# Kernel tuning notes

Measured on AMD Instinct MI355X. Metric: run time of the kernel, lower is better.

## Reference

```python
import jax, jax.numpy as jnp
import numpy as np

T, S, B, E, H = 1024, 1024, 4, 1024, 16
D = E // H          # head_dim = 64
CO = 10             # co_dim fixed in the module


def _xavier(k, shape):
    fan_out, fan_in = shape[0], shape[-1]
    s = (2.0 / (fan_in + fan_out)) ** 0.5
    return jax.random.normal(k, shape, jnp.float32) * s


def setup_inputs() -> dict:
    rng = jax.random.key(0)
    ks = jax.random.split(rng, 12)
    return {
        "query": jax.random.normal(ks[0], (T, B, E), jnp.float32),
        "key": jax.random.normal(ks[1], (S, B, E), jnp.float32),
        "value": jax.random.normal(ks[2], (S, B, E), jnp.float32),
        "in_proj_weight": _xavier(ks[3], (3 * E, E)),
        "in_proj_bias": jnp.zeros((3 * E,), jnp.float32),
        "out_proj_w": _xavier(ks[4], (E, E)),
        "out_proj_b": jnp.zeros((E,), jnp.float32),
        "co_C_q_w": _xavier(ks[5], (D, D)),
        "co_q_w": _xavier(ks[6], (CO, D)),
        "co_k_w": _xavier(ks[7], (CO, D)),
        "h_q_w": _xavier(ks[8], (1, CO)),
        "h_k_w": _xavier(ks[9], (1, CO)),
    }


def reference(query, key, value, in_proj_weight, in_proj_bias,
              out_proj_w, out_proj_b, co_C_q_w, co_q_w, co_k_w,
              h_q_w, h_k_w):
    tgt_len, bsz, embed_dim = query.shape
    src_len = key.shape[0]
    scaling = D ** (-0.5)

    Wq, Wk, Wv = jnp.split(in_proj_weight, 3, axis=0)
    bq, bk, bv = jnp.split(in_proj_bias, 3, axis=0)

    q = (query @ Wq.T + bq) * scaling                 # [T, B, E]
    k = key @ Wk.T + bk                               # [S, B, E]
    v = value @ Wv.T + bv                             # [S, B, E]

    # [T, B*H, D] -> [B*H, T, D]
    q = jnp.transpose(q.reshape(tgt_len, bsz * H, D), (1, 0, 2))
    k = jnp.transpose(k.reshape(src_len, bsz * H, D), (1, 0, 2))
    v = jnp.transpose(v.reshape(src_len, bsz * H, D), (1, 0, 2))

    # ---- co-attention gating ----
    qW = q @ co_C_q_w.T                               # [BH, T, D]
    C = jnp.tanh(jnp.einsum('btd,bsd->bts', qW, k))   # [BH, T, S]

    q2 = q @ co_q_w.T                                 # [BH, T, CO]
    k2 = k @ co_k_w.T                                 # [BH, S, CO]

    # H_q_in = q2^T + k2^T @ C^T : [BH, CO, T]
    H_q = jnp.tanh(jnp.swapaxes(q2, 1, 2) + jnp.einsum('bsc,bts->bct', k2, C))
    # H_k_in = k2^T + q2^T @ C : [BH, CO, S]
    H_k = jnp.tanh(jnp.swapaxes(k2, 1, 2) + jnp.einsum('btc,bts->bcs', q2, C))

    H_q_W = jnp.swapaxes(H_q, 1, 2) @ h_q_w.T         # [BH, T, 1]
    H_k_W = jnp.swapaxes(H_k, 1, 2) @ h_k_w.T         # [BH, S, 1]

    # NOTE: softmax over the last (size-1) axis, as in the original code;
    # this yields all-ones gates but is reproduced faithfully.
    a_q = jax.nn.softmax(H_q_W, axis=-1)              # [BH, T, 1]
    a_k = jax.nn.softmax(H_k_W, axis=-1)              # [BH, S, 1]

    q = q * a_q                                       # broadcast == repeat to D
    k = k * a_k

    # ---- standard attention ----
    attn_weights = jnp.einsum('btd,bsd->bts', q, k)   # [BH, T, S]
    attn_weights = jax.nn.softmax(attn_weights, axis=-1)
    attn = jnp.einsum('bts,bsd->btd', attn_weights, v)  # [BH, T, D]

    attn = jnp.transpose(attn, (1, 0, 2)).reshape(tgt_len, bsz, embed_dim)
    attn = attn @ out_proj_w.T + out_proj_b           # [T, B, E]

    aw = attn_weights.reshape(bsz, H, tgt_len, src_len).sum(axis=1) / H
    return attn, aw
```

## Files before the change

### kernel.cpp

```cpp
#include <hip/hip_runtime.h>

typedef __attribute__((ext_vector_type(8))) short s8v;
typedef __attribute__((ext_vector_type(4))) float f4v;
typedef unsigned short u16;

#define T_LEN 1024
#define B_SZ 4
#define H_NUM 16
#define D_DIM 64
#define E_DIM 1024

#define MBY ((size_t)1<<20)

#define OFF_X(z)     ((size_t)(z)*16*MBY)
#define OFF_AW(g)    ((size_t)(g)*16*MBY)
#define OFF_VT_HI    (32*MBY)
#define OFF_VT_LO    (40*MBY)
#define OFF_ATTN32   (48*MBY)
#define OFF_IPW_HI   (64*MBY)
#define OFF_IPW_LO   (70*MBY)
#define OFF_OPW_HI   (76*MBY)
#define OFF_OPW_LO   (78*MBY)
#define OFF_QKV(z)   ((80*MBY) + (size_t)(z)*16*MBY)
#define OFF_ATTN_HI  (80*MBY)
#define OFF_ATTN_LO  (88*MBY)

__device__ __forceinline__ u16 f2bf(float x){
    unsigned u = __float_as_uint(x);
    u += 0x7fffu + ((u>>16)&1u);
    return (u16)(u>>16);
}
__device__ __forceinline__ float bf2f(u16 h){
    return __uint_as_float(((unsigned)h)<<16);
}
__device__ __forceinline__ void glds16(const void* g, void* l){
    __builtin_amdgcn_global_load_lds((const __attribute__((address_space(1))) unsigned*)g,
                                     (__attribute__((address_space(3))) unsigned*)l, 16, 0, 0);
}
#define MFMA_BF16(a,b,c) __builtin_amdgcn_mfma_f32_16x16x32_bf16((a),(b),(c),0,0,0)

__global__ __launch_bounds__(256) void split_bf16(const float* __restrict__ src,
        u16* __restrict__ hi, u16* __restrict__ lo)
{
    size_t i = ((size_t)blockIdx.x*256 + threadIdx.x)*8;
    float4 a = *(const float4*)(src + i);
    float4 b = *(const float4*)(src + i + 4);
    float v[8] = {a.x,a.y,a.z,a.w,b.x,b.y,b.z,b.w};
    s8v hv, lv;
    #pragma unroll
    for (int j=0;j<8;++j){
        u16 h = f2bf(v[j]);
        hv[j] = (short)h;
        lv[j] = (short)f2bf(v[j] - bf2f(h));
    }
    *(s8v*)(hi+i) = hv;
    *(s8v*)(lo+i) = lv;
}

template<int MODE>
__global__ __launch_bounds__(256) void gemm_split(char* __restrict__ wsb,
        const float* __restrict__ bias0, float* __restrict__ out32)
{
    __shared__ u16 Ah[4096], Al[4096], Bh[4096], Bl[4096];
    const int tid = threadIdx.x;
    const int wv = tid>>6, l = tid&63;
    const int lr = l&15, lg = l>>4;
    const int z = (MODE==0)? blockIdx.z : 0;

    const u16 *Ahi,*Alo,*Whi,*Wlo;
    const float* bias; float scale;
    u16 *outH = nullptr, *outL = nullptr;
    if (MODE==0){
        Ahi = (const u16*)(wsb + OFF_X(z));
        Alo = Ahi + 4*MBY;
        Whi = (const u16*)(wsb + OFF_IPW_HI) + (size_t)z*E_DIM*E_DIM;
        Wlo = (const u16*)(wsb + OFF_IPW_LO) + (size_t)z*E_DIM*E_DIM;
        bias = bias0 + z*E_DIM;
        scale = (z==0)? 0.125f : 1.0f;
        outH = (u16*)(wsb + OFF_QKV(z));
        outL = outH + 4*MBY;
    } else {
        Ahi = (const u16*)(wsb + OFF_ATTN_HI);
        Alo = (const u16*)(wsb + OFF_ATTN_LO);
        Whi = (const u16*)(wsb + OFF_OPW_HI);
        Wlo = (const u16*)(wsb + OFF_OPW_LO);
        bias = bias0; scale = 1.0f;
    }

    const int m0 = blockIdx.y*128, n0 = blockIdx.x*128;

    f4v acc[4][4];
    #pragma unroll
    for (int i=0;i<4;++i)
        #pragma unroll
        for (int j=0;j<4;++j) acc[i][j] = (f4v){0.f,0.f,0.f,0.f};

    for (int k0=0; k0<E_DIM; k0+=32){
        #pragma unroll
        for (int i=0;i<2;++i){
            int ci  = i*4 + wv;
            int row = ci*16 + (l>>2);
            int u   = (l&3) ^ ((l>>2)&3);
            size_t aoff = (size_t)(m0+row)*E_DIM + k0 + u*8;
            size_t boff = (size_t)(n0+row)*E_DIM + k0 + u*8;
            glds16(Ahi+aoff, &Ah[ci*512]);
            glds16(Alo+aoff, &Al[ci*512]);
            glds16(Whi+boff, &Bh[ci*512]);
            glds16(Wlo+boff, &Bl[ci*512]);
        }
        __syncthreads();
        s8v ah[4],al[4],bh[4],bl[4];
        #pragma unroll
        for (int mi=0;mi<4;++mi){
            int row = (wv>>1)*64 + mi*16 + lr;
            int off = row*32 + ((lg ^ (row&3))<<3);
            ah[mi] = *(const s8v*)&Ah[off];
            al[mi] = *(const s8v*)&Al[off];
        }
        #pragma unroll
        for (int ni=0;ni<4;++ni){
            int row = (wv&1)*64 + ni*16 + lr;
            int off = row*32 + ((lg ^ (row&3))<<3);
            bh[ni] = *(const s8v*)&Bh[off];
            bl[ni] = *(const s8v*)&Bl[off];
        }
        #pragma unroll
        for (int mi=0;mi<4;++mi)
            #pragma unroll
            for (int ni=0;ni<4;++ni){
                acc[mi][ni] = MFMA_BF16(ah[mi], bh[ni], acc[mi][ni]);
                acc[mi][ni] = MFMA_BF16(ah[mi], bl[ni], acc[mi][ni]);
                acc[mi][ni] = MFMA_BF16(al[mi], bh[ni], acc[mi][ni]);
            }
        __syncthreads();
    }

    #pragma unroll
    for (int mi=0;mi<4;++mi){
        #pragma unroll
        for (int ni=0;ni<4;++ni){
            int n = n0 + (wv&1)*64 + ni*16 + lr;
            float bn = bias[n];
            #pragma unroll
            for (int r=0;r<4;++r){
                int m = m0 + (wv>>1)*64 + mi*16 + lg*4 + r;
                float val = (acc[mi][ni][r] + bn)*scale;
                if (MODE==0){
                    int t = m>>2, bb = m&3, hh2 = n>>6, dd = n&63;
                    size_t idx = ((size_t)(bb*H_NUM+hh2)*T_LEN + t)*D_DIM + dd;
                    u16 hb_ = f2bf(val);
                    outH[idx] = hb_;
                    outL[idx] = f2bf(val - bf2f(hb_));
                } else {
                    out32[(size_t)m*E_DIM + n] = val;
                }
            }
        }
    }
}

__global__ __launch_bounds__(256) void transpose_v(char* __restrict__ wsb)
{
    __shared__ u16 Th[64][72], Tl[64][72];
    const int tid = threadIdx.x;
    const int bh  = blockIdx.y;
    const int s0  = blockIdx.x*64;
    const u16* vh = (const u16*)(wsb + OFF_QKV(2));
    const u16* vl = vh + 4*MBY;
    u16* th = (u16*)(wsb + OFF_VT_HI);
    u16* tl = (u16*)(wsb + OFF_VT_LO);

    #pragma unroll
    for (int it=0; it<2; ++it){
        int u = it*256 + tid;
        int s = u>>3, c8 = u&7;
        size_t off = ((size_t)bh*T_LEN + s0+s)*D_DIM + c8*8;
        s8v a  = *(const s8v*)&vh[off];
        s8v b_ = *(const s8v*)&vl[off];
        #pragma unroll
        for (int j=0;j<8;++j){
            Th[c8*8+j][s] = (u16)a[j];
            Tl[c8*8+j][s] = (u16)b_[j];
        }
    }
    __syncthreads();
    #pragma unroll
    for (int it=0; it<2; ++it){
        int u = it*256 + tid;
        int d = u>>3, sc = u&7;
        s8v rh = *(const s8v*)&Th[d][sc*8];
        s8v rl = *(const s8v*)&Tl[d][sc*8];
        size_t off = ((size_t)bh*D_DIM + d)*T_LEN + s0 + sc*8;
        *(s8v*)&th[off] = rh;
        *(s8v*)&tl[off] = rl;
    }
}

__global__ __launch_bounds__(256) void attn_mfma(char* __restrict__ wsb)
{
    __shared__ u16 Ph[2][1024], Pl[2][1024];
    __shared__ float redM[16][4], redS[16][4];

    const int tid = threadIdx.x;
    const int wv = tid>>6, l = tid&63, lr = l&15, lg = l>>4;
    const int t0 = blockIdx.x*16;
    const int hg = blockIdx.y;
    const int b  = blockIdx.z;

    const u16* qhi = (const u16*)(wsb + OFF_QKV(0));
    const u16* qlo = qhi + 4*MBY;
    const u16* khi = (const u16*)(wsb + OFF_QKV(1));
    const u16* klo = khi + 4*MBY;
    const u16* vth = (const u16*)(wsb + OFF_VT_HI);
    const u16* vtl = (const u16*)(wsb + OFF_VT_LO);
    float* attn32 = (float*)(wsb + OFF_ATTN32);
    float* awb    = (float*)(wsb + OFF_AW(hg)) + (size_t)b*T_LEN*T_LEN;

    float aw[16][4];
    #pragma unroll
    for (int c=0;c<16;++c)
        #pragma unroll
        for (int r=0;r<4;++r) aw[c][r] = 0.f;

    for (int hh=0; hh<8; ++hh){
        const int h = hg*8 + hh;
        const size_t hb = (size_t)(b*H_NUM + h)*T_LEN*D_DIM;

        s8v qfh[2], qfl[2];
        #pragma unroll
        for (int kh=0;kh<2;++kh){
            size_t qo = hb + (size_t)(t0+lr)*D_DIM + kh*32 + lg*8;
            qfh[kh] = *(const s8v*)&qhi[qo];
            qfl[kh] = *(const s8v*)&qlo[qo];
        }

        f4v p[16];
        #pragma unroll
        for (int c=0;c<16;++c){
            f4v a = (f4v){0.f,0.f,0.f,0.f};
            #pragma unroll
            for (int kh=0;kh<2;++kh){
                size_t ko = hb + (size_t)(c*64 + wv*16 + lr)*D_DIM + kh*32 + lg*8;
                s8v kfh = *(const s8v*)&khi[ko];
                s8v kfl = *(const s8v*)&klo[ko];
                a = MFMA_BF16(qfh[kh], kfh, a);
                a = MFMA_BF16(qfh[kh], kfl, a);
                a = MFMA_BF16(qfl[kh], kfh, a);
            }
            p[c] = a;
        }

        float Mr[4], inv[4];
        #pragma unroll
        for (int r=0;r<4;++r){
            float m_ = p[0][r];
            #pragma unroll
            for (int c=1;c<16;++c) m_ = fmaxf(m_, p[c][r]);
            m_ = fmaxf(m_, __shfl_xor(m_,1));
            m_ = fmaxf(m_, __shfl_xor(m_,2));
            m_ = fmaxf(m_, __shfl_xor(m_,4));
            m_ = fmaxf(m_, __shfl_xor(m_,8));
            if (lr==0) redM[lg*4+r][wv] = m_;
        }
        __syncthreads();
        #pragma unroll
        for (int r=0;r<4;++r){
            float4 t4 = *(const float4*)&redM[lg*4+r][0];
            Mr[r] = fmaxf(fmaxf(t4.x,t4.y), fmaxf(t4.z,t4.w));
        }
        float sm[4] = {0.f,0.f,0.f,0.f};
        #pragma unroll
        for (int c=0;c<16;++c)
            #pragma unroll
            for (int r=0;r<4;++r){
                float e = __expf(p[c][r]-Mr[r]);
                p[c][r] = e;
                sm[r] += e;
            }
        #pragma unroll
        for (int r=0;r<4;++r){
            float s_ = sm[r];
            s_ += __shfl_xor(s_,1); s_ += __shfl_xor(s_,2);
            s_ += __shfl_xor(s_,4); s_ += __shfl_xor(s_,8);
            if (lr==0) redS[lg*4+r][wv] = s_;
        }
        __syncthreads();
        #pragma unroll
        for (int r=0;r<4;++r){
            float4 t4 = *(const float4*)&redS[lg*4+r][0];
            inv[r] = 1.0f/(t4.x+t4.y+t4.z+t4.w);
        }
        #pragma unroll
        for (int c=0;c<16;++c)
            #pragma unroll
            for (int r=0;r<4;++r){
                p[c][r] *= inv[r];
                aw[c][r] += p[c][r];
            }

        f4v O = (f4v){0.f,0.f,0.f,0.f};
        #pragma unroll
        for (int c=0;c<16;++c){
            const int pb = c&1;
            #pragma unroll
            for (int r=0;r<4;++r){
                int row = lg*4+r;
                int col = wv*16+lr;
                int idx = row*64 + (col ^ ((row&7)<<3));
                u16 hb_ = f2bf(p[c][r]);
                Ph[pb][idx] = hb_;
                Pl[pb][idx] = f2bf(p[c][r]-bf2f(hb_));
            }
            __syncthreads();
            #pragma unroll
            for (int kh=0;kh<2;++kh){
                int aidx = lr*64 + ((kh*32+lg*8) ^ ((lr&7)<<3));
                s8v pah = *(const s8v*)&Ph[pb][aidx];
                s8v pal = *(const s8v*)&Pl[pb][aidx];
                size_t vo = hb + (size_t)(wv*16+lr)*T_LEN + c*64 + kh*32 + lg*8;
                s8v vfh = *(const s8v*)&vth[vo];
                s8v vfl = *(const s8v*)&vtl[vo];
                O = MFMA_BF16(pah, vfh, O);
                O = MFMA_BF16(pah, vfl, O);
                O = MFMA_BF16(pal, vfh, O);
            }
        }
        #pragma unroll
        for (int r=0;r<4;++r){
            int m = (t0 + lg*4 + r)*B_SZ + b;
            int n = h*D_DIM + wv*16 + lr;
            attn32[(size_t)m*E_DIM + n] = O[r];
        }
    }

    #pragma unroll
    for (int c=0;c<16;++c)
        #pragma unroll
        for (int r=0;r<4;++r){
            int t = t0 + lg*4 + r;
            awb[(size_t)t*T_LEN + c*64 + wv*16 + lr] = aw[c][r];
        }
}

__global__ __launch_bounds__(256) void aw_reduce2(const float* __restrict__ p0,
        const float* __restrict__ p1, float* __restrict__ out2)
{
    size_t i = ((size_t)blockIdx.x*256 + threadIdx.x)*4;
    float4 a = *(const float4*)(p0+i);
    float4 b = *(const float4*)(p1+i);
    float4 r;
    r.x = (a.x+b.x)*0.0625f;
    r.y = (a.y+b.y)*0.0625f;
    r.z = (a.z+b.z)*0.0625f;
    r.w = (a.w+b.w)*0.0625f;
    *(float4*)(out2+i) = r;
}

extern "C" void kernel_launch(void* const* d_in, const int* in_sizes, int n_in,
                              void* d_out, int out_size, void* d_ws, size_t ws_size,
                              hipStream_t stream) {
    const float* query = (const float*)d_in[0];
    const float* key   = (const float*)d_in[1];
    const float* value = (const float*)d_in[2];
    const float* ipw   = (const float*)d_in[3];
    const float* ipb   = (const float*)d_in[4];
    const float* opw   = (const float*)d_in[5];
    const float* opb   = (const float*)d_in[6];

    char* wsb = (char*)d_ws;
    float* out = (float*)d_out;

    split_bf16<<<2048,256,0,stream>>>(query, (u16*)(wsb+OFF_X(0)), (u16*)(wsb+OFF_X(0))+4*MBY);
    split_bf16<<<2048,256,0,stream>>>(key,   (u16*)(wsb+OFF_X(1)), (u16*)(wsb+OFF_X(1))+4*MBY);
    split_bf16<<<2048,256,0,stream>>>(value, (u16*)(wsb+OFF_X(2)), (u16*)(wsb+OFF_X(2))+4*MBY);
    split_bf16<<<1536,256,0,stream>>>(ipw,   (u16*)(wsb+OFF_IPW_HI), (u16*)(wsb+OFF_IPW_LO));
    split_bf16<<< 512,256,0,stream>>>(opw,   (u16*)(wsb+OFF_OPW_HI), (u16*)(wsb+OFF_OPW_LO));
    gemm_split<0><<<dim3(8,32,3),256,0,stream>>>(wsb, ipb, nullptr);
    transpose_v<<<dim3(16,64),256,0,stream>>>(wsb);
    attn_mfma<<<dim3(64,2,4),256,0,stream>>>(wsb);
    split_bf16<<<2048,256,0,stream>>>((const float*)(wsb+OFF_ATTN32),
                                      (u16*)(wsb+OFF_ATTN_HI), (u16*)(wsb+OFF_ATTN_LO));
    gemm_split<1><<<dim3(8,32,1),256,0,stream>>>(wsb, opb, out);
    aw_reduce2<<<4096,256,0,stream>>>((const float*)(wsb+OFF_AW(0)),
                                      (const float*)(wsb+OFF_AW(1)), out + 4*MBY);
}
```

Measured before the change: 688.0 us.

## Restructure attention kernel to 8 waves with full-row P staging and fused bf16 split

The attention kernel moves from 4 to 8 waves per block. Each wave computes half as many score columns, and a single combined max/sum exchange replaces the two separate reductions. The whole 16x1024 probability tile is staged in LDS with one barrier instead of a barrier per 64-column chunk. The PV product is split across two wave halves over the key dimension and reduced through LDS. The attention output is written directly as hi/lo bf16, which removes the separate split kernel and its fp32 round trip. In exchange it uses much more LDS (about 64KB), which may limit occupancy, and it adds an extra cross-wave reduction.

After: 637.7 us. 1.08x faster.

```diff
diff --git a/kernel.cpp b/kernel.cpp
--- a/kernel.cpp
+++ b/kernel.cpp
@@ -16,14 +16,13 @@
 #define OFF_AW(g)    ((size_t)(g)*16*MBY)
 #define OFF_VT_HI    (32*MBY)
 #define OFF_VT_LO    (40*MBY)
-#define OFF_ATTN32   (48*MBY)
+#define OFF_ATTN_HI  (48*MBY)
+#define OFF_ATTN_LO  (56*MBY)
 #define OFF_IPW_HI   (64*MBY)
 #define OFF_IPW_LO   (70*MBY)
 #define OFF_OPW_HI   (76*MBY)
 #define OFF_OPW_LO   (78*MBY)
 #define OFF_QKV(z)   ((80*MBY) + (size_t)(z)*16*MBY)
-#define OFF_ATTN_HI  (80*MBY)
-#define OFF_ATTN_LO  (88*MBY)
 
 __device__ __forceinline__ u16 f2bf(float x){
     unsigned u = __float_as_uint(x);
@@ -196,13 +195,15 @@
     }
 }
 
-__global__ __launch_bounds__(256) void attn_mfma(char* __restrict__ wsb)
+__global__ __launch_bounds__(512,4) void attn_mfma(char* __restrict__ wsb)
 {
-    __shared__ u16 Ph[2][1024], Pl[2][1024];
-    __shared__ float redM[16][4], redS[16][4];
+    __shared__ u16 Ph[16384], Pl[16384];
+    __shared__ float Ored[16*68];
+    __shared__ float redMS[16*16];
 
     const int tid = threadIdx.x;
     const int wv = tid>>6, l = tid&63, lr = l&15, lg = l>>4;
+    const int sh = wv>>2, dq = wv&3;
     const int t0 = blockIdx.x*16;
     const int hg = blockIdx.y;
     const int b  = blockIdx.z;
@@ -213,14 +214,13 @@
     const u16* klo = khi + 4*MBY;
     const u16* vth = (const u16*)(wsb + OFF_VT_HI);
     const u16* vtl = (const u16*)(wsb + OFF_VT_LO);
-    float* attn32 = (float*)(wsb + OFF_ATTN32);
-    float* awb    = (float*)(wsb + OFF_AW(hg)) + (size_t)b*T_LEN*T_LEN;
-
-    float aw[16][4];
-    #pragma unroll
-    for (int c=0;c<16;++c)
-        #pragma unroll
-        for (int r=0;r<4;++r) aw[c][r] = 0.f;
+    u16* attnH = (u16*)(wsb + OFF_ATTN_HI);
+    u16* attnL = (u16*)(wsb + OFF_ATTN_LO);
+    float* awb = (float*)(wsb + OFF_AW(hg)) + (size_t)b*T_LEN*T_LEN;
+
+    f4v aw[8];
+    #pragma unroll
+    for (int c=0;c<8;++c) aw[c] = (f4v){0.f,0.f,0.f,0.f};
 
     for (int hh=0; hh<8; ++hh){
         const int h = hg*8 + hh;
@@ -234,111 +234,140 @@
             qfl[kh] = *(const s8v*)&qlo[qo];
         }
 
-        f4v p[16];
-        #pragma unroll
-        for (int c=0;c<16;++c){
+        f4v p[8];
+        const size_t kb = hb + (size_t)(wv*16+lr)*D_DIM + lg*8;
+        #pragma unroll
+        for (int c2=0;c2<8;++c2){
             f4v a = (f4v){0.f,0.f,0.f,0.f};
             #pragma unroll
             for (int kh=0;kh<2;++kh){
-                size_t ko = hb + (size_t)(c*64 + wv*16 + lr)*D_DIM + kh*32 + lg*8;
+                size_t ko = kb + (size_t)c2*8192 + kh*32;
                 s8v kfh = *(const s8v*)&khi[ko];
                 s8v kfl = *(const s8v*)&klo[ko];
                 a = MFMA_BF16(qfh[kh], kfh, a);
                 a = MFMA_BF16(qfh[kh], kfl, a);
                 a = MFMA_BF16(qfl[kh], kfh, a);
             }
-            p[c] = a;
-        }
-
-        float Mr[4], inv[4];
+            p[c2] = a;
+        }
+
+        float mw[4];
         #pragma unroll
         for (int r=0;r<4;++r){
             float m_ = p[0][r];
             #pragma unroll
-            for (int c=1;c<16;++c) m_ = fmaxf(m_, p[c][r]);
+            for (int c2=1;c2<8;++c2) m_ = fmaxf(m_, p[c2][r]);
             m_ = fmaxf(m_, __shfl_xor(m_,1));
             m_ = fmaxf(m_, __shfl_xor(m_,2));
             m_ = fmaxf(m_, __shfl_xor(m_,4));
             m_ = fmaxf(m_, __shfl_xor(m_,8));
-            if (lr==0) redM[lg*4+r][wv] = m_;
+            float sw = 0.f;
+            #pragma unroll
+            for (int c2=0;c2<8;++c2){
+                float e = __expf(p[c2][r]-m_);
+                p[c2][r] = e;
+                sw += e;
+            }
+            sw += __shfl_xor(sw,1); sw += __shfl_xor(sw,2);
+            sw += __shfl_xor(sw,4); sw += __shfl_xor(sw,8);
+            mw[r] = m_;
+            if (lr==0){
+                redMS[(lg*4+r)*16 + wv*2]     = m_;
+                redMS[(lg*4+r)*16 + wv*2 + 1] = sw;
+            }
         }
         __syncthreads();
+        float scl[4];
         #pragma unroll
         for (int r=0;r<4;++r){
-            float4 t4 = *(const float4*)&redM[lg*4+r][0];
-            Mr[r] = fmaxf(fmaxf(t4.x,t4.y), fmaxf(t4.z,t4.w));
-        }
-        float sm[4] = {0.f,0.f,0.f,0.f};
-        #pragma unroll
-        for (int c=0;c<16;++c)
+            const float* rp = &redMS[(lg*4+r)*16];
+            f4v x0 = *(const f4v*)&rp[0];
+            f4v x1 = *(const f4v*)&rp[4];
+            f4v x2 = *(const f4v*)&rp[8];
+            f4v x3 = *(const f4v*)&rp[12];
+            float M = fmaxf(fmaxf(fmaxf(x0[0],x0[2]), fmaxf(x1[0],x1[2])),
+                            fmaxf(fmaxf(x2[0],x2[2]), fmaxf(x3[0],x3[2])));
+            float S = x0[1]*__expf(x0[0]-M) + x0[3]*__expf(x0[2]-M)
+                    + x1[1]*__expf(x1[0]-M) + x1[3]*__expf(x1[2]-M)
+                    + x2[1]*__expf(x2[0]-M) + x2[3]*__expf(x2[2]-M)
+                    + x3[1]*__expf(x3[0]-M) + x3[3]*__expf(x3[2]-M);
+            scl[r] = __expf(mw[r]-M)/S;
+        }
+
+        #pragma unroll
+        for (int c2=0;c2<8;++c2){
             #pragma unroll
             for (int r=0;r<4;++r){
-                float e = __expf(p[c][r]-Mr[r]);
-                p[c][r] = e;
-                sm[r] += e;
-            }
-        #pragma unroll
-        for (int r=0;r<4;++r){
-            float s_ = sm[r];
-            s_ += __shfl_xor(s_,1); s_ += __shfl_xor(s_,2);
-            s_ += __shfl_xor(s_,4); s_ += __shfl_xor(s_,8);
-            if (lr==0) redS[lg*4+r][wv] = s_;
+                float v = p[c2][r]*scl[r];
+                aw[c2][r] += v;
+                int row  = lg*4 + r;
+                int colS = c2*128 + wv*16 + lr;
+                int addr = row*1024 + (((colS>>3) ^ row)<<3) + (colS&7);
+                u16 hb_ = f2bf(v);
+                Ph[addr] = hb_;
+                Pl[addr] = f2bf(v - bf2f(hb_));
+            }
         }
         __syncthreads();
-        #pragma unroll
-        for (int r=0;r<4;++r){
-            float4 t4 = *(const float4*)&redS[lg*4+r][0];
-            inv[r] = 1.0f/(t4.x+t4.y+t4.z+t4.w);
-        }
-        #pragma unroll
-        for (int c=0;c<16;++c)
-            #pragma unroll
-            for (int r=0;r<4;++r){
-                p[c][r] *= inv[r];
-                aw[c][r] += p[c][r];
-            }
-
-        f4v O = (f4v){0.f,0.f,0.f,0.f};
-        #pragma unroll
-        for (int c=0;c<16;++c){
-            const int pb = c&1;
-            #pragma unroll
-            for (int r=0;r<4;++r){
-                int row = lg*4+r;
-                int col = wv*16+lr;
-                int idx = row*64 + (col ^ ((row&7)<<3));
-                u16 hb_ = f2bf(p[c][r]);
-                Ph[pb][idx] = hb_;
-                Pl[pb][idx] = f2bf(p[c][r]-bf2f(hb_));
-            }
-            __syncthreads();
-            #pragma unroll
-            for (int kh=0;kh<2;++kh){
-                int aidx = lr*64 + ((kh*32+lg*8) ^ ((lr&7)<<3));
-                s8v pah = *(const s8v*)&Ph[pb][aidx];
-                s8v pal = *(const s8v*)&Pl[pb][aidx];
-                size_t vo = hb + (size_t)(wv*16+lr)*T_LEN + c*64 + kh*32 + lg*8;
+
+        f4v O0 = (f4v){0.f,0.f,0.f,0.f};
+        f4v O1 = (f4v){0.f,0.f,0.f,0.f};
+        const size_t vb = hb + (size_t)(dq*16+lr)*T_LEN + lg*8;
+        __builtin_amdgcn_s_setprio(1);
+        #pragma unroll
+        for (int k2=0;k2<8;++k2){
+            {
+                int ks = sh*16 + k2*2;
+                int pa = lr*1024 + (((ks*4+lg) ^ lr)<<3);
+                s8v pah = *(const s8v*)&Ph[pa];
+                s8v pal = *(const s8v*)&Pl[pa];
+                size_t vo = vb + (size_t)ks*32;
                 s8v vfh = *(const s8v*)&vth[vo];
                 s8v vfl = *(const s8v*)&vtl[vo];
-                O = MFMA_BF16(pah, vfh, O);
-                O = MFMA_BF16(pah, vfl, O);
-                O = MFMA_BF16(pal, vfh, O);
-            }
-        }
-        #pragma unroll
-        for (int r=0;r<4;++r){
-            int m = (t0 + lg*4 + r)*B_SZ + b;
-            int n = h*D_DIM + wv*16 + lr;
-            attn32[(size_t)m*E_DIM + n] = O[r];
-        }
-    }
-
-    #pragma unroll
-    for (int c=0;c<16;++c)
+                O0 = MFMA_BF16(pah, vfh, O0);
+                O0 = MFMA_BF16(pah, vfl, O0);
+                O0 = MFMA_BF16(pal, vfh, O0);
+            }
+            {
+                int ks = sh*16 + k2*2 + 1;
+                int pa = lr*1024 + (((ks*4+lg) ^ lr)<<3);
+                s8v pah = *(const s8v*)&Ph[pa];
+                s8v pal = *(const s8v*)&Pl[pa];
+                size_t vo = vb + (size_t)ks*32;
+                s8v vfh = *(const s8v*)&vth[vo];
+                s8v vfl = *(const s8v*)&vtl[vo];
+                O1 = MFMA_BF16(pah, vfh, O1);
+                O1 = MFMA_BF16(pah, vfl, O1);
+                O1 = MFMA_BF16(pal, vfh, O1);
+            }
+        }
+        __builtin_amdgcn_s_setprio(0);
+
+        if (sh==1){
+            #pragma unroll
+            for (int r=0;r<4;++r)
+                Ored[(lg*4+r)*68 + dq*16+lr] = O0[r]+O1[r];
+        }
+        __syncthreads();
+        if (sh==0){
+            #pragma unroll
+            for (int r=0;r<4;++r){
+                float val = O0[r]+O1[r] + Ored[(lg*4+r)*68 + dq*16+lr];
+                int m = (t0 + lg*4 + r)*B_SZ + b;
+                size_t oi = (size_t)m*E_DIM + h*D_DIM + dq*16 + lr;
+                u16 hb_ = f2bf(val);
+                attnH[oi] = hb_;
+                attnL[oi] = f2bf(val - bf2f(hb_));
+            }
+        }
+    }
+
+    #pragma unroll
+    for (int c2=0;c2<8;++c2)
         #pragma unroll
         for (int r=0;r<4;++r){
             int t = t0 + lg*4 + r;
-            awb[(size_t)t*T_LEN + c*64 + wv*16 + lr] = aw[c][r];
+            awb[(size_t)t*T_LEN + c2*128 + wv*16 + lr] = aw[c2][r];
         }
 }
 
@@ -377,9 +406,7 @@
     split_bf16<<< 512,256,0,stream>>>(opw,   (u16*)(wsb+OFF_OPW_HI), (u16*)(wsb+OFF_OPW_LO));
     gemm_split<0><<<dim3(8,32,3),256,0,stream>>>(wsb, ipb, nullptr);
     transpose_v<<<dim3(16,64),256,0,stream>>>(wsb);
-    attn_mfma<<<dim3(64,2,4),256,0,stream>>>(wsb);
-    split_bf16<<<2048,256,0,stream>>>((const float*)(wsb+OFF_ATTN32),
-                                      (u16*)(wsb+OFF_ATTN_HI), (u16*)(wsb+OFF_ATTN_LO));
+    attn_mfma<<<dim3(64,2,4),512,0,stream>>>(wsb);
     gemm_split<1><<<dim3(8,32,1),256,0,stream>>>(wsb, opb, out);
     aw_reduce2<<<4096,256,0,stream>>>((const float*)(wsb+OFF_AW(0)),
                                       (const float*)(wsb+OFF_AW(1)), out + 4*MBY);
```

## Restructure attention kernel with LDS-staged K/V pipeline and fused epilogues

Applied to the files above, without the earlier changes.

Rewrites the attention kernel so each 512-thread block owns one batch and a 16-query tile across all 16 heads. Each wave handles a 128-key slice, and K/V tiles are staged into LDS with async global_load_lds double buffering plus manual waitcnt and scheduling barriers. Softmax becomes a split reduction across waves, with the P·V partial results combined through LDS atomics. The attention output is written straight as bf16 hi/lo, and the head-averaged weights are written straight to the output, which removes the separate split and aw_reduce kernels and the fp32 intermediates. This adds heavy LDS use (about 80KB per block), fragile hand-written vmcnt accounting, and more atomics.

Result: faster. 604.5 us (-12.1%).

```diff
diff --git a/kernel.cpp b/kernel.cpp
--- a/kernel.cpp
+++ b/kernel.cpp
@@ -2,6 +2,7 @@
 
 typedef __attribute__((ext_vector_type(8))) short s8v;
 typedef __attribute__((ext_vector_type(4))) float f4v;
+typedef __attribute__((ext_vector_type(4))) unsigned u32x4;
 typedef unsigned short u16;
 
 #define T_LEN 1024
@@ -13,17 +14,15 @@
 #define MBY ((size_t)1<<20)
 
 #define OFF_X(z)     ((size_t)(z)*16*MBY)
-#define OFF_AW(g)    ((size_t)(g)*16*MBY)
 #define OFF_VT_HI    (32*MBY)
 #define OFF_VT_LO    (40*MBY)
-#define OFF_ATTN32   (48*MBY)
+#define OFF_ATTN_HI  (48*MBY)
+#define OFF_ATTN_LO  (56*MBY)
 #define OFF_IPW_HI   (64*MBY)
 #define OFF_IPW_LO   (70*MBY)
 #define OFF_OPW_HI   (76*MBY)
 #define OFF_OPW_LO   (78*MBY)
 #define OFF_QKV(z)   ((80*MBY) + (size_t)(z)*16*MBY)
-#define OFF_ATTN_HI  (80*MBY)
-#define OFF_ATTN_LO  (88*MBY)
 
 __device__ __forceinline__ u16 f2bf(float x){
     unsigned u = __float_as_uint(x);
@@ -38,6 +37,11 @@
                                      (__attribute__((address_space(3))) unsigned*)l, 16, 0, 0);
 }
 #define MFMA_BF16(a,b,c) __builtin_amdgcn_mfma_f32_16x16x32_bf16((a),(b),(c),0,0,0)
+#define SCHED_WALL __builtin_amdgcn_sched_barrier(0)
+#define VM_WAIT8 asm volatile("s_waitcnt vmcnt(8)" ::: "memory")
+#define VM_WAIT0 asm volatile("s_waitcnt vmcnt(0)" ::: "memory")
+#define LGKM0    asm volatile("s_waitcnt lgkmcnt(0)" ::: "memory")
+#define BARRIER() do{ SCHED_WALL; LGKM0; __builtin_amdgcn_s_barrier(); SCHED_WALL; }while(0)
 
 __global__ __launch_bounds__(256) void split_bf16(const float* __restrict__ src,
         u16* __restrict__ hi, u16* __restrict__ lo)
@@ -196,16 +200,19 @@
     }
 }
 
-__global__ __launch_bounds__(256) void attn_mfma(char* __restrict__ wsb)
+__global__ __launch_bounds__(512,2) void attn_mfma(char* __restrict__ wsb,
+        float* __restrict__ aw_out)
 {
-    __shared__ u16 Ph[2][1024], Pl[2][1024];
-    __shared__ float redM[16][4], redS[16][4];
+    __shared__ u16 STG[8][2][4096];
+    __shared__ unsigned PEX[8][512];
+    __shared__ float ORED[2][1024];
+    __shared__ float REDMS[16][16];
 
     const int tid = threadIdx.x;
     const int wv = tid>>6, l = tid&63, lr = l&15, lg = l>>4;
     const int t0 = blockIdx.x*16;
-    const int hg = blockIdx.y;
-    const int b  = blockIdx.z;
+    const int b  = blockIdx.y;
+    const int sb = wv*128;
 
     const u16* qhi = (const u16*)(wsb + OFF_QKV(0));
     const u16* qlo = qhi + 4*MBY;
@@ -213,147 +220,211 @@
     const u16* klo = khi + 4*MBY;
     const u16* vth = (const u16*)(wsb + OFF_VT_HI);
     const u16* vtl = (const u16*)(wsb + OFF_VT_LO);
-    float* attn32 = (float*)(wsb + OFF_ATTN32);
-    float* awb    = (float*)(wsb + OFF_AW(hg)) + (size_t)b*T_LEN*T_LEN;
-
-    float aw[16][4];
-    #pragma unroll
-    for (int c=0;c<16;++c)
-        #pragma unroll
-        for (int r=0;r<4;++r) aw[c][r] = 0.f;
-
-    for (int hh=0; hh<8; ++hh){
-        const int h = hg*8 + hh;
-        const size_t hb = (size_t)(b*H_NUM + h)*T_LEN*D_DIM;
+    u16* attnH = (u16*)(wsb + OFF_ATTN_HI);
+    u16* attnL = (u16*)(wsb + OFF_ATTN_LO);
+
+    *(f4v*)&((float*)ORED)[tid*4] = (f4v){0.f,0.f,0.f,0.f};
+
+    f4v aw[4][2];
+    #pragma unroll
+    for (int bk=0;bk<4;++bk){ aw[bk][0]=(f4v){0,0,0,0}; aw[bk][1]=(f4v){0,0,0,0}; }
+
+    u16* sA = &STG[wv][0][0];
+    u16* sB = &STG[wv][1][0];
+    unsigned* ex = &PEX[wv][0];
+
+    auto stageK = [&](u16* slot, size_t hb_, int sbase){
+        #pragma unroll
+        for (int i=0;i<4;++i){
+            int sl = i*8 + (l>>3);
+            int gu = (l&7) ^ (sl&7);
+            size_t src = hb_ + (size_t)(sbase+sl)*64 + gu*8;
+            glds16(khi + src, slot + i*512);
+            glds16(klo + src, slot + 2048 + i*512);
+        }
+    };
+    auto stageV = [&](u16* slot, size_t vb_, int sbase){
+        #pragma unroll
+        for (int i=0;i<4;++i){
+            int d = i*16 + (l>>2);
+            int gu = ((l&3) + (d>>2)) & 3;
+            size_t src = vb_ + (size_t)d*1024 + sbase + gu*8;
+            glds16(vth + src, slot + i*512);
+            glds16(vtl + src, slot + 2048 + i*512);
+        }
+    };
+
+    {
+        size_t hb0 = (size_t)(b*H_NUM)*65536;
+        stageK(sA, hb0, sb);
+        stageK(sB, hb0, sb+32);
+    }
+
+    for (int hh=0; hh<16; ++hh){
+        const size_t hb  = (size_t)(b*H_NUM + hh)*65536;
+        const size_t hbn = (size_t)(b*H_NUM + ((hh+1)&15))*65536;
 
         s8v qfh[2], qfl[2];
         #pragma unroll
         for (int kh=0;kh<2;++kh){
-            size_t qo = hb + (size_t)(t0+lr)*D_DIM + kh*32 + lg*8;
+            size_t qo = hb + (size_t)(t0+lr)*64 + kh*32 + lg*8;
             qfh[kh] = *(const s8v*)&qhi[qo];
             qfl[kh] = *(const s8v*)&qlo[qo];
         }
 
-        f4v p[16];
-        #pragma unroll
-        for (int c=0;c<16;++c){
-            f4v a = (f4v){0.f,0.f,0.f,0.f};
-            #pragma unroll
-            for (int kh=0;kh<2;++kh){
-                size_t ko = hb + (size_t)(c*64 + wv*16 + lr)*D_DIM + kh*32 + lg*8;
-                s8v kfh = *(const s8v*)&khi[ko];
-                s8v kfl = *(const s8v*)&klo[ko];
-                a = MFMA_BF16(qfh[kh], kfh, a);
-                a = MFMA_BF16(qfh[kh], kfl, a);
-                a = MFMA_BF16(qfl[kh], kfh, a);
+        f4v p[4][2];
+        #pragma unroll
+        for (int bk=0;bk<4;++bk){
+            SCHED_WALL;
+            if (bk==1) stageK(sA, hb, sb+64);
+            else if (bk==2) stageK(sB, hb, sb+96);
+            else if (bk==3) stageV(sA, hb, sb);
+            VM_WAIT8; SCHED_WALL;
+            const u16* sp = (bk&1)? sB : sA;
+            #pragma unroll
+            for (int t=0;t<2;++t){
+                int sl = t*16 + lr;
+                int sw = sl&7;
+                s8v k0h = *(const s8v*)&sp[sl*64 + ((lg  ^sw)<<3)];
+                s8v k1h = *(const s8v*)&sp[sl*64 + (((4+lg)^sw)<<3)];
+                s8v k0l = *(const s8v*)&sp[2048 + sl*64 + ((lg  ^sw)<<3)];
+                s8v k1l = *(const s8v*)&sp[2048 + sl*64 + (((4+lg)^sw)<<3)];
+                f4v a1 = (f4v){0,0,0,0}, a2 = (f4v){0,0,0,0};
+                a1 = MFMA_BF16(k0h, qfh[0], a1);
+                a1 = MFMA_BF16(k1h, qfh[1], a1);
+                a2 = MFMA_BF16(k0h, qfl[0], a2);
+                a2 = MFMA_BF16(k1h, qfl[1], a2);
+                a2 = MFMA_BF16(k0l, qfh[0], a2);
+                a2 = MFMA_BF16(k1l, qfh[1], a2);
+                p[bk][t] = a1 + a2;
             }
-            p[c] = a;
-        }
-
-        float Mr[4], inv[4];
-        #pragma unroll
-        for (int r=0;r<4;++r){
-            float m_ = p[0][r];
-            #pragma unroll
-            for (int c=1;c<16;++c) m_ = fmaxf(m_, p[c][r]);
-            m_ = fmaxf(m_, __shfl_xor(m_,1));
-            m_ = fmaxf(m_, __shfl_xor(m_,2));
-            m_ = fmaxf(m_, __shfl_xor(m_,4));
-            m_ = fmaxf(m_, __shfl_xor(m_,8));
-            if (lr==0) redM[lg*4+r][wv] = m_;
-        }
-        __syncthreads();
-        #pragma unroll
-        for (int r=0;r<4;++r){
-            float4 t4 = *(const float4*)&redM[lg*4+r][0];
-            Mr[r] = fmaxf(fmaxf(t4.x,t4.y), fmaxf(t4.z,t4.w));
-        }
-        float sm[4] = {0.f,0.f,0.f,0.f};
-        #pragma unroll
-        for (int c=0;c<16;++c)
-            #pragma unroll
-            for (int r=0;r<4;++r){
-                float e = __expf(p[c][r]-Mr[r]);
-                p[c][r] = e;
-                sm[r] += e;
+        }
+        SCHED_WALL;
+        stageV(sB, hb, sb+32);
+
+        float mw = p[0][0][0];
+        #pragma unroll
+        for (int bk=0;bk<4;++bk)
+            #pragma unroll
+            for (int t=0;t<2;++t)
+                #pragma unroll
+                for (int r=0;r<4;++r) mw = fmaxf(mw, p[bk][t][r]);
+        mw = fmaxf(mw, __shfl_xor(mw, 16));
+        mw = fmaxf(mw, __shfl_xor(mw, 32));
+        float sw_ = 0.f;
+        #pragma unroll
+        for (int bk=0;bk<4;++bk)
+            #pragma unroll
+            for (int t=0;t<2;++t)
+                #pragma unroll
+                for (int r=0;r<4;++r){
+                    float e = __expf(p[bk][t][r] - mw);
+                    p[bk][t][r] = e;
+                    sw_ += e;
+                }
+        sw_ += __shfl_xor(sw_, 16);
+        sw_ += __shfl_xor(sw_, 32);
+        if (lg==0){ REDMS[lr][wv*2] = mw; REDMS[lr][wv*2+1] = sw_; }
+        BARRIER();
+        float scl;
+        {
+            f4v x0 = *(const f4v*)&REDMS[lr][0];
+            f4v x1 = *(const f4v*)&REDMS[lr][4];
+            f4v x2 = *(const f4v*)&REDMS[lr][8];
+            f4v x3 = *(const f4v*)&REDMS[lr][12];
+            float M = fmaxf(fmaxf(fmaxf(x0[0],x0[2]), fmaxf(x1[0],x1[2])),
+                            fmaxf(fmaxf(x2[0],x2[2]), fmaxf(x3[0],x3[2])));
+            float S = x0[1]*__expf(x0[0]-M) + x0[3]*__expf(x0[2]-M)
+                    + x1[1]*__expf(x1[0]-M) + x1[3]*__expf(x1[2]-M)
+                    + x2[1]*__expf(x2[0]-M) + x2[3]*__expf(x2[2]-M)
+                    + x3[1]*__expf(x3[0]-M) + x3[3]*__expf(x3[2]-M);
+            scl = __expf(mw - M) / S;
+        }
+
+        u32x4 pk[4][2];
+        #pragma unroll
+        for (int bk=0;bk<4;++bk)
+            #pragma unroll
+            for (int t=0;t<2;++t){
+                float v0 = p[bk][t][0]*scl, v1 = p[bk][t][1]*scl;
+                float v2 = p[bk][t][2]*scl, v3 = p[bk][t][3]*scl;
+                aw[bk][t][0] += v0; aw[bk][t][1] += v1;
+                aw[bk][t][2] += v2; aw[bk][t][3] += v3;
+                u16 h0=f2bf(v0), h1=f2bf(v1), h2=f2bf(v2), h3=f2bf(v3);
+                u16 l0=f2bf(v0-bf2f(h0)), l1=f2bf(v1-bf2f(h1));
+                u16 l2=f2bf(v2-bf2f(h2)), l3=f2bf(v3-bf2f(h3));
+                pk[bk][t] = (u32x4){ (unsigned)h0 | ((unsigned)h1<<16),
+                                     (unsigned)h2 | ((unsigned)h3<<16),
+                                     (unsigned)l0 | ((unsigned)l1<<16),
+                                     (unsigned)l2 | ((unsigned)l3<<16) };
             }
-        #pragma unroll
-        for (int r=0;r<4;++r){
-            float s_ = sm[r];
-            s_ += __shfl_xor(s_,1); s_ += __shfl_xor(s_,2);
-            s_ += __shfl_xor(s_,4); s_ += __shfl_xor(s_,8);
-            if (lr==0) redS[lg*4+r][wv] = s_;
-        }
-        __syncthreads();
-        #pragma unroll
-        for (int r=0;r<4;++r){
-            float4 t4 = *(const float4*)&redS[lg*4+r][0];
-            inv[r] = 1.0f/(t4.x+t4.y+t4.z+t4.w);
-        }
-        #pragma unroll
-        for (int c=0;c<16;++c)
-            #pragma unroll
-            for (int r=0;r<4;++r){
-                p[c][r] *= inv[r];
-                aw[c][r] += p[c][r];
+
+        f4v Oa[4], Ob[4];
+        #pragma unroll
+        for (int ds=0;ds<4;++ds){ Oa[ds]=(f4v){0,0,0,0}; Ob[ds]=(f4v){0,0,0,0}; }
+        #pragma unroll
+        for (int bk=0;bk<4;++bk){
+            SCHED_WALL;
+            if (bk==1) stageV(sA, hb, sb+64);
+            else if (bk==2) stageV(sB, hb, sb+96);
+            else if (bk==3) stageK(sA, hbn, sb);
+            VM_WAIT8; SCHED_WALL;
+            *(u32x4*)&ex[l*8]   = pk[bk][0];
+            *(u32x4*)&ex[l*8+4] = pk[bk][1];
+            int srcA = ((lg&1)*32 + lr)*8 + (lg>>1)*4;
+            u32x4 rdA = *(const u32x4*)&ex[srcA];
+            u32x4 rdB = *(const u32x4*)&ex[srcA + 128];
+            union Wu { unsigned u[4]; s8v s; } uh, ul;
+            uh.u[0]=rdA[0]; uh.u[1]=rdA[1]; uh.u[2]=rdB[0]; uh.u[3]=rdB[1];
+            ul.u[0]=rdA[2]; ul.u[1]=rdA[3]; ul.u[2]=rdB[2]; ul.u[3]=rdB[3];
+            const u16* vp = (bk&1)? sB : sA;
+            #pragma unroll
+            for (int ds=0;ds<4;++ds){
+                int d = ds*16 + lr;
+                int uu = (lg - (d>>2)) & 3;
+                s8v vh_ = *(const s8v*)&vp[d*32 + (uu<<3)];
+                s8v vl_ = *(const s8v*)&vp[2048 + d*32 + (uu<<3)];
+                Oa[ds] = MFMA_BF16(uh.s, vh_, Oa[ds]);
+                Ob[ds] = MFMA_BF16(uh.s, vl_, Ob[ds]);
+                Ob[ds] = MFMA_BF16(ul.s, vh_, Ob[ds]);
             }
-
-        f4v O = (f4v){0.f,0.f,0.f,0.f};
-        #pragma unroll
-        for (int c=0;c<16;++c){
-            const int pb = c&1;
-            #pragma unroll
-            for (int r=0;r<4;++r){
-                int row = lg*4+r;
-                int col = wv*16+lr;
-                int idx = row*64 + (col ^ ((row&7)<<3));
-                u16 hb_ = f2bf(p[c][r]);
-                Ph[pb][idx] = hb_;
-                Pl[pb][idx] = f2bf(p[c][r]-bf2f(hb_));
-            }
-            __syncthreads();
-            #pragma unroll
-            for (int kh=0;kh<2;++kh){
-                int aidx = lr*64 + ((kh*32+lg*8) ^ ((lr&7)<<3));
-                s8v pah = *(const s8v*)&Ph[pb][aidx];
-                s8v pal = *(const s8v*)&Pl[pb][aidx];
-                size_t vo = hb + (size_t)(wv*16+lr)*T_LEN + c*64 + kh*32 + lg*8;
-                s8v vfh = *(const s8v*)&vth[vo];
-                s8v vfl = *(const s8v*)&vtl[vo];
-                O = MFMA_BF16(pah, vfh, O);
-                O = MFMA_BF16(pah, vfl, O);
-                O = MFMA_BF16(pal, vfh, O);
-            }
-        }
-        #pragma unroll
-        for (int r=0;r<4;++r){
-            int m = (t0 + lg*4 + r)*B_SZ + b;
-            int n = h*D_DIM + wv*16 + lr;
-            attn32[(size_t)m*E_DIM + n] = O[r];
-        }
-    }
-
-    #pragma unroll
-    for (int c=0;c<16;++c)
-        #pragma unroll
-        for (int r=0;r<4;++r){
-            int t = t0 + lg*4 + r;
-            awb[(size_t)t*T_LEN + c*64 + wv*16 + lr] = aw[c][r];
-        }
-}
-
-__global__ __launch_bounds__(256) void aw_reduce2(const float* __restrict__ p0,
-        const float* __restrict__ p1, float* __restrict__ out2)
-{
-    size_t i = ((size_t)blockIdx.x*256 + threadIdx.x)*4;
-    float4 a = *(const float4*)(p0+i);
-    float4 b = *(const float4*)(p1+i);
-    float4 r;
-    r.x = (a.x+b.x)*0.0625f;
-    r.y = (a.y+b.y)*0.0625f;
-    r.z = (a.z+b.z)*0.0625f;
-    r.w = (a.w+b.w)*0.0625f;
-    *(float4*)(out2+i) = r;
+        }
+        SCHED_WALL;
+        stageK(sB, hbn, sb+32);
+
+        #pragma unroll
+        for (int ds=0;ds<4;++ds)
+            #pragma unroll
+            for (int r=0;r<4;++r)
+                atomicAdd(&ORED[hh&1][(lg*4+r)*64 + ds*16 + lr], Oa[ds][r]+Ob[ds][r]);
+        BARRIER();
+        {
+            int e = tid*2;
+            float v0 = ORED[hh&1][e], v1 = ORED[hh&1][e+1];
+            ORED[hh&1][e] = 0.f; ORED[hh&1][e+1] = 0.f;
+            int qq = e>>6, dd = e&63;
+            size_t oi = ((size_t)((t0+qq)*B_SZ + b))*E_DIM + hh*64 + dd;
+            u16 h0 = f2bf(v0), h1 = f2bf(v1);
+            *(unsigned*)&attnH[oi] = (unsigned)h0 | ((unsigned)h1<<16);
+            u16 lo0 = f2bf(v0 - bf2f(h0)), lo1 = f2bf(v1 - bf2f(h1));
+            *(unsigned*)&attnL[oi] = (unsigned)lo0 | ((unsigned)lo1<<16);
+        }
+    }
+
+    VM_WAIT0; SCHED_WALL;
+    float* awt = (float*)&STG[wv][0][0];
+    #pragma unroll
+    for (int bk=0;bk<4;++bk)
+        #pragma unroll
+        for (int t=0;t<2;++t)
+            *(f4v*)&awt[lr*128 + bk*32 + t*16 + lg*4] = aw[bk][t]*0.0625f;
+    #pragma unroll
+    for (int j=0;j<8;++j){
+        int idx = j*256 + l*4;
+        f4v vv = *(const f4v*)&awt[idx];
+        *(f4v*)&aw_out[(size_t)b*(T_LEN*T_LEN) + (size_t)(t0+(idx>>7))*T_LEN
+                       + sb + (idx&127)] = vv;
+    }
 }
 
 extern "C" void kernel_launch(void* const* d_in, const int* in_sizes, int n_in,
@@ -377,10 +448,6 @@
     split_bf16<<< 512,256,0,stream>>>(opw,   (u16*)(wsb+OFF_OPW_HI), (u16*)(wsb+OFF_OPW_LO));
     gemm_split<0><<<dim3(8,32,3),256,0,stream>>>(wsb, ipb, nullptr);
     transpose_v<<<dim3(16,64),256,0,stream>>>(wsb);
-    attn_mfma<<<dim3(64,2,4),256,0,stream>>>(wsb);
-    split_bf16<<<2048,256,0,stream>>>((const float*)(wsb+OFF_ATTN32),
-                                      (u16*)(wsb+OFF_ATTN_HI), (u16*)(wsb+OFF_ATTN_LO));
+    attn_mfma<<<dim3(64,4),512,0,stream>>>(wsb, out + (size_t)B_SZ*T_LEN*E_DIM/1);
     gemm_split<1><<<dim3(8,32,1),256,0,stream>>>(wsb, opb, out);
-    aw_reduce2<<<4096,256,0,stream>>>((const float*)(wsb+OFF_AW(0)),
-                                      (const float*)(wsb+OFF_AW(1)), out + 4*MBY);
-}
+}
```
